# Kernel tuning notes

Hardware: AMD Instinct MI355X
Metric: run time of the kernel (lower is better)

The kernel has to match this reference:

```python
import jax, jax.numpy as jnp
import numpy as np

N_SRC = 50000
N_TGT = 50000
E = 320000
D = 256          # feature dim == hidden_channels
H = 256
OUT = 16
L = 2
P_DROP = 0.1
NEG_SLOPE = 0.01  # F.leaky_relu default


def _seg_mean(x, src_idx, dst_idx, n_dst):
    # gather source features along edges, mean-aggregate per destination (PyG SAGE default aggr='mean')
    msgs = x[src_idx]                                            # [E, D]
    s = jax.ops.segment_sum(msgs, dst_idx, num_segments=n_dst)   # [n_dst, D]
    cnt = jax.ops.segment_sum(jnp.ones((dst_idx.shape[0],), x.dtype), dst_idx, num_segments=n_dst)
    return s / jnp.maximum(cnt, 1.0)[:, None]


def _dropout(x, p, key):
    keep = jax.random.bernoulli(key, 1.0 - p, x.shape)
    return jnp.where(keep, x / (1.0 - p), jnp.zeros((), x.dtype))


def setup_inputs() -> dict:
    key = jax.random.key(0)
    ks = jax.random.split(key, 16)
    sc_in = 1.0 / np.sqrt(D)
    sc_h = 1.0 / np.sqrt(H)
    inp = {
        'x_source': jax.random.normal(ks[0], (N_SRC, D), jnp.float32),
        'x_target': jax.random.normal(ks[1], (N_TGT, D), jnp.float32),
        'ei_st': jax.random.randint(ks[2], (2, E), 0, N_SRC, jnp.int32),  # row0: source idx, row1: target idx
        'ei_ts': jax.random.randint(ks[3], (2, E), 0, N_TGT, jnp.int32),  # row0: target idx, row1: source idx
        # SAGEConv params per layer per relation; lin_l has bias, lin_r does not (PyG)
        'Wl_st': jax.random.normal(ks[4], (L, D, H), jnp.float32) * sc_in,
        'Wr_st': jax.random.normal(ks[5], (L, D, H), jnp.float32) * sc_in,
        'b_st': jnp.zeros((L, H), jnp.float32),
        'Wl_ts': jax.random.normal(ks[6], (L, D, H), jnp.float32) * sc_in,
        'Wr_ts': jax.random.normal(ks[7], (L, D, H), jnp.float32) * sc_in,
        'b_ts': jnp.zeros((L, H), jnp.float32),
        'Wout': jax.random.normal(ks[8], (H, OUT), jnp.float32) * sc_h,
        'bout': jnp.zeros((OUT,), jnp.float32),
    }
    return inp


def reference(x_source, x_target, ei_st, ei_ts, Wl_st, Wr_st, b_st, Wl_ts, Wr_ts, b_ts, Wout, bout):
    drop_key = jax.random.key(42)
    x_s, x_t = x_source, x_target
    for l in range(L):
        # relation ('source','edge','target'): messages source -> target
        m_t = _seg_mean(x_s, ei_st[0], ei_st[1], N_TGT)
        new_t = m_t @ Wl_st[l] + b_st[l] + x_t @ Wr_st[l]
        # relation ('target','rev_edge','source'): messages target -> source
        m_s = _seg_mean(x_t, ei_ts[0], ei_ts[1], N_SRC)
        new_s = m_s @ Wl_ts[l] + b_ts[l] + x_s @ Wr_ts[l]
        # leaky_relu + dropout (F.dropout default training=True)
        new_s = jnp.where(new_s >= 0, new_s, NEG_SLOPE * new_s)
        new_t = jnp.where(new_t >= 0, new_t, NEG_SLOPE * new_t)
        x_s = _dropout(new_s, P_DROP, jax.random.fold_in(drop_key, 2 * l))
        x_t = _dropout(new_t, P_DROP, jax.random.fold_in(drop_key, 2 * l + 1))
    return x_s @ Wout + bout  # [N_SRC, OUT]
```

## Files before the change

kernel.cpp:

```cpp
#include <hip/hip_runtime.h>
#include <stdint.h>

#define NSRC 50000
#define NTGT 50000
#define NE   320000
#define DIN  256
#define HID  256
#define DOUT 16

#define GBM 64
#define GBLK ((NSRC + GBM - 1) / GBM)
#define MASK_DW_PER (GBLK * 512)

typedef __attribute__((ext_vector_type(8))) short bf16x8;
typedef __attribute__((ext_vector_type(4))) float f32x4;
typedef __attribute__((ext_vector_type(4))) uint u32x4;

__device__ inline ushort f2b(float f) {
  uint32_t u = __float_as_uint(f);
  return (ushort)((u + 0x7FFFu + ((u >> 16) & 1u)) >> 16);
}
__device__ inline float b2f(ushort h) { return __uint_as_float(((uint32_t)h) << 16); }

typedef __attribute__((address_space(3))) uint32_t lds_u32_t;
typedef const __attribute__((address_space(1))) uint32_t glb_u32_t;
__device__ __forceinline__ void ld_lds16(const ushort* g, ushort* lds) {
  __builtin_amdgcn_global_load_lds((glb_u32_t*)g, (lds_u32_t*)lds, 16, 0, 0);
}

__host__ __device__ constexpr uint64_t tf2x32(uint32_t k0, uint32_t k1,
                                              uint32_t x0, uint32_t x1) {
  uint32_t ks2 = k0 ^ k1 ^ 0x1BD11BDAu;
  x0 += k0; x1 += k1;
#define TF_ROT(x, r) (((x) << (r)) | ((x) >> (32 - (r))))
#define TF_RND(r) { x0 += x1; x1 = TF_ROT(x1, r) ^ x0; }
  TF_RND(13) TF_RND(15) TF_RND(26) TF_RND(6)
  x0 += k1;  x1 += ks2 + 1u;
  TF_RND(17) TF_RND(29) TF_RND(16) TF_RND(24)
  x0 += ks2; x1 += k0 + 2u;
  TF_RND(13) TF_RND(15) TF_RND(26) TF_RND(6)
  x0 += k0;  x1 += k1 + 3u;
  TF_RND(17) TF_RND(29) TF_RND(16) TF_RND(24)
  x0 += k1;  x1 += ks2 + 4u;
  TF_RND(13) TF_RND(15) TF_RND(26) TF_RND(6)
  x0 += ks2; x1 += k0 + 5u;
#undef TF_RND
#undef TF_ROT
  return (uint64_t(x0) << 32) | uint64_t(x1);
}

constexpr uint64_t FOLD[4] = {
  tf2x32(0u, 42u, 0u, 0u),
  tf2x32(0u, 42u, 0u, 1u),
  tf2x32(0u, 42u, 0u, 2u),
  tf2x32(0u, 42u, 0u, 3u),
};

__device__ __forceinline__ void mask_word(uint32_t* __restrict__ masks, int d) {
  int g = d / MASK_DW_PER;
  int w = d - g * MASK_DW_PER;
  int gt = w >> 1, half = w & 1;
  int gblk = gt >> 8, gtid = gt & 255;
  int wave = gtid >> 6, lane = gtid & 63;
  int q = lane >> 4, r = lane & 15;
  uint64_t fk = (g == 0) ? FOLD[1] : (g == 1 ? FOLD[0] : FOLD[2]);
  uint32_t kk0 = (uint32_t)(fk >> 32), kk1 = (uint32_t)fk;
  int mbase = gblk * GBM;
  uint32_t mword = 0;
#pragma unroll
  for (int bb = 0; bb < 32; ++bb) {
    int s = half * 32 + bb;
    int si = s >> 4, se = (s >> 2) & 3, sj = s & 3;
    uint32_t rowg = (uint32_t)(mbase + si * 16 + q * 4 + se);
    uint32_t colg = (uint32_t)(wave * 64 + sj * 16 + r);
    uint64_t rr = tf2x32(kk0, kk1, 0u, rowg * 256u + colg);
    uint32_t bits = (uint32_t)(rr >> 32) ^ (uint32_t)rr;
    mword |= (((bits >> 9) < 7549747u) ? 1u : 0u) << bb;
  }
  masks[d] = mword;
}

#define NB_CVT  25000
#define NB_W    96
#define NB_HIST 2500
#define PREP_T  (NB_CVT + NB_W + NB_HIST)

struct PrepArgs {
  const float *xs, *xt;
  ushort *oxs, *oxt;
  const float* wsrc[6];
  ushort* wdst[6];
  const int *ei_a, *ei_b;
  int *cur_a, *cur_b;
};

__global__ __launch_bounds__(256) void prep_kernel(PrepArgs p) {
  __shared__ ushort tile[64][65];
  int blk = (int)(((long long)blockIdx.x * 97) % PREP_T);
  int tid = threadIdx.x;
  if (blk < NB_CVT) {
    const float* in = blk < (NB_CVT / 2) ? p.xs : p.xt;
    ushort* out = blk < (NB_CVT / 2) ? p.oxs : p.oxt;
    int i = (blk % (NB_CVT / 2)) * 256 + tid;
    float4 v = ((const float4*)in)[i];
    ushort4 o;
    o.x = f2b(v.x); o.y = f2b(v.y); o.z = f2b(v.z); o.w = f2b(v.w);
    ((ushort4*)out)[i] = o;
    return;
  }
  blk -= NB_CVT;
  if (blk < NB_W) {
    const float* W = p.wsrc[blk >> 4];
    ushort* Wt = p.wdst[blk >> 4];
    int ktile = (blk >> 2) & 3, ntile = blk & 3;
#pragma unroll
    for (int rep = 0; rep < 16; ++rep) {
      int lin = rep * 256 + tid;
      int kk = lin >> 6, nn = lin & 63;
      tile[nn][kk] = f2b(W[(size_t)(ktile * 64 + kk) * 256 + ntile * 64 + nn]);
    }
    __syncthreads();
#pragma unroll
    for (int rep = 0; rep < 16; ++rep) {
      int lin = rep * 256 + tid;
      int nn = lin >> 6, kk = lin & 63;
      Wt[(size_t)(ntile * 64 + nn) * 256 + ktile * 64 + kk] = tile[nn][kk];
    }
    return;
  }
  blk -= NB_W;
  const int* ei = blk < (NB_HIST / 2) ? p.ei_a : p.ei_b;
  int* cur = blk < (NB_HIST / 2) ? p.cur_a : p.cur_b;
  int e = (blk % (NB_HIST / 2)) * 256 + tid;
  if (e < NE) atomicAdd(cur + ei[NE + e], 1);
}

#define SB 1024
__global__ __launch_bounds__(SB) void scan_partial(const int* __restrict__ cur_a,
                                                   const int* __restrict__ cur_b,
                                                   int* __restrict__ bsum,
                                                   int n, int nbPer) {
  __shared__ int red[SB];
  int b = blockIdx.x;
  const int* cnt = b < nbPer ? cur_a : cur_b;
  int i = (b % nbPer) * SB + threadIdx.x;
  red[threadIdx.x] = (i < n) ? cnt[i] : 0;
  __syncthreads();
  for (int d = SB / 2; d > 0; d >>= 1) {
    if (threadIdx.x < d) red[threadIdx.x] += red[threadIdx.x + d];
    __syncthreads();
  }
  if (threadIdx.x == 0) bsum[b] = red[0];
}

__global__ __launch_bounds__(128) void scan_base(int* __restrict__ bsum, int nbPer) {
  __shared__ int buf[2][64];
  int half = threadIdx.x >> 6;
  int t = threadIdx.x & 63;
  buf[half][t] = (t < nbPer) ? bsum[half * nbPer + t] : 0;
  __syncthreads();
  for (int d = 1; d < 64; d <<= 1) {
    int v = (t >= d) ? buf[half][t - d] : 0;
    __syncthreads();
    buf[half][t] += v;
    __syncthreads();
  }
  if (t < nbPer) bsum[half * nbPer + t] = (t == 0) ? 0 : buf[half][t - 1];
}

__global__ __launch_bounds__(SB) void scan_final(int* __restrict__ cur_a,
                                                 int* __restrict__ cur_b,
                                                 int* __restrict__ offs_a,
                                                 int* __restrict__ offs_b,
                                                 const int* __restrict__ bsum,
                                                 int n, int nbPer) {
  __shared__ int part[SB];
  int b = blockIdx.x;
  bool first = b < nbPer;
  int* cur = first ? cur_a : cur_b;
  int* offs = first ? offs_a : offs_b;
  int i = (b % nbPer) * SB + threadIdx.x;
  int v = (i < n) ? cur[i] : 0;
  part[threadIdx.x] = v;
  __syncthreads();
  for (int d = 1; d < SB; d <<= 1) {
    int tv = (threadIdx.x >= d) ? part[threadIdx.x - d] : 0;
    __syncthreads();
    part[threadIdx.x] += tv;
    __syncthreads();
  }
  int excl = part[threadIdx.x] - v + bsum[b];
  if (i < n) {
    offs[i] = excl;
    cur[i] = 0;
  }
  if (i == n - 1) offs[n] = excl + v;
}

__global__ __launch_bounds__(256) void csr_fill2(const int* __restrict__ ei_a,
                                                 const int* __restrict__ ei_b,
                                                 const int* __restrict__ offs_a,
                                                 const int* __restrict__ offs_b,
                                                 int* __restrict__ cur_a,
                                                 int* __restrict__ cur_b,
                                                 int* __restrict__ adj_a,
                                                 int* __restrict__ adj_b,
                                                 int nE, int nbPer) {
  int blk = blockIdx.x;
  bool first = blk < nbPer;
  const int* ei = first ? ei_a : ei_b;
  const int* offs = first ? offs_a : offs_b;
  int* cur = first ? cur_a : cur_b;
  int* adj = first ? adj_a : adj_b;
  int e = (blk % nbPer) * 256 + threadIdx.x;
  if (e >= nE) return;
  int dst = ei[nE + e];
  int pos = atomicAdd(cur + dst, 1);
  adj[offs[dst] + pos] = ei[e];
}

__device__ __forceinline__ void gather_row8(const ushort* __restrict__ x,
                                            const int* __restrict__ offs,
                                            const int* __restrict__ adj,
                                            ushort* __restrict__ m,
                                            int row, int lane) {
  int start = offs[row], end = offs[row + 1];
  float a0 = 0.f, a1 = 0.f, a2 = 0.f, a3 = 0.f;
  float a4 = 0.f, a5 = 0.f, a6 = 0.f, a7 = 0.f;
  const ushort* xb = x + lane * 8;
  int e = start;
  for (; e + 3 < end; e += 4) {
    int s0 = adj[e], s1 = adj[e + 1], s2 = adj[e + 2], s3 = adj[e + 3];
    u32x4 v0 = *(const u32x4*)(xb + (size_t)s0 * DIN);
    u32x4 v1 = *(const u32x4*)(xb + (size_t)s1 * DIN);
    u32x4 v2 = *(const u32x4*)(xb + (size_t)s2 * DIN);
    u32x4 v3 = *(const u32x4*)(xb + (size_t)s3 * DIN);
    const ushort* u;
    u = (const ushort*)&v0;
    a0 += b2f(u[0]); a1 += b2f(u[1]); a2 += b2f(u[2]); a3 += b2f(u[3]);
    a4 += b2f(u[4]); a5 += b2f(u[5]); a6 += b2f(u[6]); a7 += b2f(u[7]);
    u = (const ushort*)&v1;
    a0 += b2f(u[0]); a1 += b2f(u[1]); a2 += b2f(u[2]); a3 += b2f(u[3]);
    a4 += b2f(u[4]); a5 += b2f(u[5]); a6 += b2f(u[6]); a7 += b2f(u[7]);
    u = (const ushort*)&v2;
    a0 += b2f(u[0]); a1 += b2f(u[1]); a2 += b2f(u[2]); a3 += b2f(u[3]);
    a4 += b2f(u[4]); a5 += b2f(u[5]); a6 += b2f(u[6]); a7 += b2f(u[7]);
    u = (const ushort*)&v3;
    a0 += b2f(u[0]); a1 += b2f(u[1]); a2 += b2f(u[2]); a3 += b2f(u[3]);
    a4 += b2f(u[4]); a5 += b2f(u[5]); a6 += b2f(u[6]); a7 += b2f(u[7]);
  }
  for (; e < end; ++e) {
    int s = adj[e];
    u32x4 v = *(const u32x4*)(xb + (size_t)s * DIN);
    const ushort* u = (const ushort*)&v;
    a0 += b2f(u[0]); a1 += b2f(u[1]); a2 += b2f(u[2]); a3 += b2f(u[3]);
    a4 += b2f(u[4]); a5 += b2f(u[5]); a6 += b2f(u[6]); a7 += b2f(u[7]);
  }
  float inv = 1.0f / fmaxf((float)(end - start), 1.0f);
  ushort o[8];
  o[0] = f2b(a0 * inv); o[1] = f2b(a1 * inv); o[2] = f2b(a2 * inv); o[3] = f2b(a3 * inv);
  o[4] = f2b(a4 * inv); o[5] = f2b(a5 * inv); o[6] = f2b(a6 * inv); o[7] = f2b(a7 * inv);
  *(u32x4*)(m + (size_t)row * DIN + lane * 8) = *(const u32x4*)o;
}

#define GG_GB 6250
#define G2_MASKB (2 * MASK_DW_PER / 256)
#define GM_T (GG_GB + G2_MASKB)

__global__ __launch_bounds__(256) void gather_mask_h(
    const ushort* __restrict__ x, const int* __restrict__ offs,
    const int* __restrict__ adj, ushort* __restrict__ m,
    uint32_t* __restrict__ masks, int nRows) {
  int blk = (int)(((long long)blockIdx.x * 97) % GM_T);
  int tid = threadIdx.x;
  if (blk >= GG_GB) {
    mask_word(masks, (blk - GG_GB) * 256 + tid);
    return;
  }
  int row = blk * 8 + (tid >> 5);
  if (row < nRows) gather_row8(x, offs, adj, m, row, tid & 31);
}

__device__ __forceinline__ void gemm_kloop(
    int bid, const ushort* __restrict__ A1, const ushort* __restrict__ A2,
    const ushort* __restrict__ W1t, const ushort* __restrict__ W2t,
    int M, ushort* sA, ushort* sB, f32x4 acc[4][4]) {
  const int tid = threadIdx.x;
  const int wave = tid >> 6, lane = tid & 63;
  const int q = lane >> 4, r = lane & 15;
  const int mbase = bid * GBM;

  const int arow = tid >> 2;
  const int akc = (tid & 3) * 8;
  const int agrow = min(mbase + arow, M - 1);
  const ushort* a1p = A1 + (size_t)agrow * DIN + akc;
  const ushort* a2p = A2 + (size_t)agrow * DIN + akc;
  const ushort* w1b = W1t + (size_t)arow * DIN + akc;
  const ushort* w2b = W2t + (size_t)arow * DIN + akc;
  ushort* ldsA0 = sA + wave * 512;
  ushort* ldsA1 = sA + 2048 + wave * 512;

#pragma unroll
  for (int t = 0; t < 8; ++t) {
    const int kt = t * 32;
    __syncthreads();
    ld_lds16(a1p + kt, ldsA0);
    ld_lds16(a2p + kt, ldsA1);
#pragma unroll
    for (int c = 0; c < 4; ++c) {
      ld_lds16(w1b + c * (64 * DIN) + kt, sB + c * 2048 + wave * 512);
      ld_lds16(w2b + c * (64 * DIN) + kt, sB + 8192 + c * 2048 + wave * 512);
    }
    __syncthreads();
#pragma unroll
    for (int ph = 0; ph < 2; ++ph) {
      bf16x8 af[4], bfr[4];
#pragma unroll
      for (int i = 0; i < 4; ++i)
        af[i] = *(const bf16x8*)&sA[ph * 2048 + (i * 16 + r) * 32 + q * 8];
#pragma unroll
      for (int j = 0; j < 4; ++j)
        bfr[j] = *(const bf16x8*)&sB[ph * 8192 + (wave * 64 + j * 16 + r) * 32 + q * 8];
#pragma unroll
      for (int i = 0; i < 4; ++i)
#pragma unroll
        for (int j = 0; j < 4; ++j)
          acc[i][j] = __builtin_amdgcn_mfma_f32_16x16x32_bf16(af[i], bfr[j],
                                                              acc[i][j], 0, 0, 0);
    }
  }
}

__device__ __forceinline__ void gemm_body(
    int bid, const ushort* __restrict__ A1, const ushort* __restrict__ A2,
    const ushort* __restrict__ W1t, const ushort* __restrict__ W2t,
    const float* __restrict__ bias, const uint2* __restrict__ mk,
    ushort* __restrict__ C, int M, ushort* sA, ushort* sB) {
  const int tid = threadIdx.x;
  const int wave = tid >> 6, lane = tid & 63;
  const int q = lane >> 4, r = lane & 15;
  const int mbase = bid * GBM;
  const uint2 km = mk[bid * 256 + tid];

  f32x4 acc[4][4] = {};
  gemm_kloop(bid, A1, A2, W1t, W2t, M, sA, sB, acc);

  float bj[4];
#pragma unroll
  for (int j = 0; j < 4; ++j) bj[j] = bias[wave * 64 + j * 16 + r];
#pragma unroll
  for (int i = 0; i < 4; ++i) {
#pragma unroll
    for (int e = 0; e < 4; ++e) {
      int rowg = mbase + i * 16 + q * 4 + e;
      if (rowg >= M) continue;
#pragma unroll
      for (int j = 0; j < 4; ++j) {
        const int s = i * 16 + e * 4 + j;
        int colg = wave * 64 + j * 16 + r;
        float v = acc[i][j][e] + bj[j];
        v = v >= 0.0f ? v : 0.01f * v;
        uint32_t keep = ((s < 32 ? km.x >> s : km.y >> (s - 32)) & 1u);
        v = keep ? v * (1.0f / 0.9f) : 0.0f;
        C[(size_t)rowg * HID + colg] = f2b(v);
      }
    }
  }
}

__global__ __launch_bounds__(256, 4) void gemm_dual_mfma(
    const ushort* __restrict__ A1, const ushort* __restrict__ A2,
    const ushort* __restrict__ W1t, const ushort* __restrict__ W2t,
    const float* __restrict__ bias, const uint2* __restrict__ mk,
    ushort* __restrict__ C, int M) {
  __shared__ ushort sA[2][GBM * 32];
  __shared__ ushort sB[2][HID * 32];
  gemm_body(blockIdx.x, A1, A2, W1t, W2t, bias, mk, C, M, &sA[0][0], &sB[0][0]);
}

#define G1_T (GBLK + GG_GB)

__global__ __launch_bounds__(256, 4) void gemm1_gather(
    const ushort* __restrict__ A1, const ushort* __restrict__ A2,
    const ushort* __restrict__ W1t, const ushort* __restrict__ W2t,
    const float* __restrict__ bias, const uint2* __restrict__ mk,
    ushort* __restrict__ C, int M,
    const ushort* __restrict__ gx, const int* __restrict__ goffs,
    const int* __restrict__ gadj, ushort* __restrict__ gm, int gRows) {
  __shared__ ushort sA[2][GBM * 32];
  __shared__ ushort sB[2][HID * 32];
  int blk = (int)(((long long)blockIdx.x * 101) % G1_T);
  if (blk < GBLK) {
    gemm_body(blk, A1, A2, W1t, W2t, bias, mk, C, M, &sA[0][0], &sB[0][0]);
  } else {
    int row = (blk - GBLK) * 8 + (threadIdx.x >> 5);
    if (row < gRows) gather_row8(gx, goffs, gadj, gm, row, threadIdx.x & 31);
  }
}

#define GG_MASKB (MASK_DW_PER / 256)
#define GG_T  (GBLK + GG_GB + GG_MASKB)

__global__ __launch_bounds__(256, 4) void gemm_gather(
    const ushort* __restrict__ A1, const ushort* __restrict__ A2,
    const ushort* __restrict__ W1t, const ushort* __restrict__ W2t,
    const float* __restrict__ bias, const uint2* __restrict__ mk,
    ushort* __restrict__ C, int M,
    const ushort* __restrict__ gx, const int* __restrict__ goffs,
    const int* __restrict__ gadj, ushort* __restrict__ gm, int gRows,
    uint32_t* __restrict__ masks) {
  __shared__ ushort sA[2][GBM * 32];
  __shared__ ushort sB[2][HID * 32];
  int blk = (int)(((long long)blockIdx.x * 101) % GG_T);
  if (blk < GBLK) {
    gemm_body(blk, A1, A2, W1t, W2t, bias, mk, C, M, &sA[0][0], &sB[0][0]);
  } else if (blk < GBLK + GG_GB) {
    int row = (blk - GBLK) * 8 + (threadIdx.x >> 5);
    if (row < gRows) gather_row8(gx, goffs, gadj, gm, row, threadIdx.x & 31);
  } else {
    mask_word(masks,
              2 * MASK_DW_PER + (blk - GBLK - GG_GB) * 256 + (int)threadIdx.x);
  }
}

__global__ __launch_bounds__(256) void out_gemm_h(const ushort* __restrict__ X,
                                                  const float* __restrict__ Wout,
                                                  const float* __restrict__ bout,
                                                  float* __restrict__ C, int M) {
  __shared__ float sW[DIN * DOUT];
  int tid = threadIdx.x;
#pragma unroll
  for (int i = 0; i < (DIN * DOUT) / 256; ++i) sW[i * 256 + tid] = Wout[i * 256 + tid];
  __syncthreads();
  int rr = tid >> 4, c = tid & 15;
  int row = blockIdx.x * 16 + rr;
  if (row >= M) return;
  float acc = bout[c];
  const ushort* xp = X + (size_t)row * DIN;
  for (int k = 0; k < DIN; k += 8) {
    uint4 u = *(const uint4*)(xp + k);
    const ushort* us = (const ushort*)&u;
#pragma unroll
    for (int t = 0; t < 8; ++t) acc += b2f(us[t]) * sW[(k + t) * DOUT + c];
  }
  C[(size_t)row * DOUT + c] = acc;
}

extern "C" void kernel_launch(void* const* d_in, const int* in_sizes, int n_in,
                              void* d_out, int out_size, void* d_ws, size_t ws_size,
                              hipStream_t stream) {
  const float* x_source = (const float*)d_in[0];
  const float* x_target = (const float*)d_in[1];
  const int* ei_st = (const int*)d_in[2];
  const int* ei_ts = (const int*)d_in[3];
  const float* Wl_st = (const float*)d_in[4];
  const float* Wr_st = (const float*)d_in[5];
  const float* b_st  = (const float*)d_in[6];
  const float* Wl_ts = (const float*)d_in[7];
  const float* Wr_ts = (const float*)d_in[8];
  const float* b_ts  = (const float*)d_in[9];
  const float* Wout  = (const float*)d_in[10];
  const float* bout  = (const float*)d_in[11];
  float* out = (float*)d_out;

  const size_t F = (size_t)NSRC * DIN;
  const size_t WM = (size_t)DIN * HID;
  const int nbScan = (NSRC + SB - 1) / SB;
  const size_t intCount = (NTGT + 1) + (NSRC + 1) + 2 * NE + NTGT + NSRC +
                          2 * nbScan + 3 * MASK_DW_PER;
  const size_t need = (5 * F + 6 * WM) * sizeof(ushort) + intCount * sizeof(int);
  if (ws_size < need) return;

  ushort* xs0h = (ushort*)d_ws;
  ushort* xt0h = xs0h + F;
  ushort* B0h  = xt0h + F;
  ushort* B1h  = B0h + F;
  ushort* B2h  = B1h + F;
  ushort* wt0  = B2h + F;
  ushort* wt1  = wt0 + WM;
  ushort* wt2  = wt1 + WM;
  ushort* wt3  = wt2 + WM;
  ushort* wt4  = wt3 + WM;
  ushort* wt5  = wt4 + WM;
  int* ip      = (int*)(wt5 + WM);
  int* offs_st = ip;
  int* offs_ts = offs_st + NTGT + 1;
  int* adj_st  = offs_ts + NSRC + 1;
  int* adj_ts  = adj_st + NE;
  int* cur_t   = adj_ts + NE;
  int* cur_s   = cur_t + NTGT;
  int* bsum    = cur_s + NSRC;
  uint32_t* masks = (uint32_t*)(bsum + 2 * nbScan);

  const int EB = (NE + 255) / 256;

  (void)hipMemsetAsync(cur_t, 0, (NTGT + NSRC) * sizeof(int), stream);
  PrepArgs pa;
  pa.xs = x_source; pa.xt = x_target; pa.oxs = xs0h; pa.oxt = xt0h;
  pa.wsrc[0] = Wl_st;      pa.wdst[0] = wt0;
  pa.wsrc[1] = Wr_st;      pa.wdst[1] = wt1;
  pa.wsrc[2] = Wl_ts;      pa.wdst[2] = wt2;
  pa.wsrc[3] = Wr_ts;      pa.wdst[3] = wt3;
  pa.wsrc[4] = Wl_ts + WM; pa.wdst[4] = wt4;
  pa.wsrc[5] = Wr_ts + WM; pa.wdst[5] = wt5;
  pa.ei_a = ei_st; pa.ei_b = ei_ts;
  pa.cur_a = cur_t; pa.cur_b = cur_s;
  prep_kernel<<<PREP_T, 256, 0, stream>>>(pa);

  scan_partial<<<2 * nbScan, SB, 0, stream>>>(cur_t, cur_s, bsum, NTGT, nbScan);
  scan_base<<<1, 128, 0, stream>>>(bsum, nbScan);
  scan_final<<<2 * nbScan, SB, 0, stream>>>(cur_t, cur_s, offs_st, offs_ts,
                                            bsum, NTGT, nbScan);
  csr_fill2<<<2 * EB, 256, 0, stream>>>(ei_st, ei_ts, offs_st, offs_ts,
                                        cur_t, cur_s, adj_st, adj_ts, NE, EB);

  gather_mask_h<<<GM_T, 256, 0, stream>>>(xs0h, offs_st, adj_st, B0h,
                                          masks, NTGT);

  gemm1_gather<<<G1_T, 256, 0, stream>>>(
      B0h, xt0h, wt0, wt1, b_st, (const uint2*)(masks), B2h, NTGT,
      xt0h, offs_ts, adj_ts, B1h, NSRC);

  gemm_gather<<<GG_T, 256, 0, stream>>>(
      B1h, xs0h, wt2, wt3, b_ts, (const uint2*)(masks + MASK_DW_PER), B0h, NSRC,
      B2h, offs_ts, adj_ts, xt0h, NSRC, masks);

  gemm_dual_mfma<<<GBLK, 256, 0, stream>>>(
      xt0h, B0h, wt4, wt5, b_ts + HID, (const uint2*)(masks + 2 * MASK_DW_PER),
      B2h, NSRC);

  out_gemm_h<<<(NSRC + 15) / 16, 256, 0, stream>>>(B2h, Wout, bout, out, NSRC);
}
```

Measured before the change: 442.2 us.

## Fuse neighbor gather and dropout mask generation into SAGE GEMM kernels

Each GEMM block now gathers and mean-aggregates its own 64 rows into a global bounce buffer, then runs the dual GEMM on it. It also computes its dropout mask bits inline instead of reading a precomputed mask buffer. Layer-1 dropout for the target side is skipped, since the final output depends only on source features. This cuts the launches from four to two, removes the mask buffer, and lets the two layer-1 relations run in one grid. The cost is that blocks now serialize gather latency before the MFMA loop, and the gather no longer overlaps GEMM work done by other blocks within a launch.

```diff
diff --git a/kernel.cpp b/kernel.cpp
--- a/kernel.cpp
+++ b/kernel.cpp
@@ -10,7 +10,6 @@
 
 #define GBM 64
 #define GBLK ((NSRC + GBM - 1) / GBM)
-#define MASK_DW_PER (GBLK * 512)
 
 typedef __attribute__((ext_vector_type(8))) short bf16x8;
 typedef __attribute__((ext_vector_type(4))) float f32x4;
@@ -56,28 +55,24 @@
   tf2x32(0u, 42u, 0u, 3u),
 };
 
-__device__ __forceinline__ void mask_word(uint32_t* __restrict__ masks, int d) {
-  int g = d / MASK_DW_PER;
-  int w = d - g * MASK_DW_PER;
-  int gt = w >> 1, half = w & 1;
-  int gblk = gt >> 8, gtid = gt & 255;
-  int wave = gtid >> 6, lane = gtid & 63;
-  int q = lane >> 4, r = lane & 15;
+__device__ __forceinline__ uint2 mask_pair(int g, int bid, int wave, int q, int r) {
   uint64_t fk = (g == 0) ? FOLD[1] : (g == 1 ? FOLD[0] : FOLD[2]);
   uint32_t kk0 = (uint32_t)(fk >> 32), kk1 = (uint32_t)fk;
-  int mbase = gblk * GBM;
-  uint32_t mword = 0;
-#pragma unroll
-  for (int bb = 0; bb < 32; ++bb) {
-    int s = half * 32 + bb;
+  int mbase = bid * GBM;
+  uint32_t kmx = 0, kmy = 0;
+#pragma unroll 2
+  for (int s = 0; s < 64; ++s) {
     int si = s >> 4, se = (s >> 2) & 3, sj = s & 3;
     uint32_t rowg = (uint32_t)(mbase + si * 16 + q * 4 + se);
     uint32_t colg = (uint32_t)(wave * 64 + sj * 16 + r);
     uint64_t rr = tf2x32(kk0, kk1, 0u, rowg * 256u + colg);
     uint32_t bits = (uint32_t)(rr >> 32) ^ (uint32_t)rr;
-    mword |= (((bits >> 9) < 7549747u) ? 1u : 0u) << bb;
-  }
-  masks[d] = mword;
+    uint32_t b = ((bits >> 9) < 7549747u) ? 1u : 0u;
+    if (s < 32) kmx |= b << s;
+    else        kmy |= b << (s - 32);
+  }
+  uint2 km; km.x = kmx; km.y = kmy;
+  return km;
 }
 
 #define NB_CVT  25000
@@ -219,10 +214,10 @@
   adj[offs[dst] + pos] = ei[e];
 }
 
-__device__ __forceinline__ void gather_row8(const ushort* __restrict__ x,
+__device__ __forceinline__ void gather_row8(const ushort* x,
                                             const int* __restrict__ offs,
                                             const int* __restrict__ adj,
-                                            ushort* __restrict__ m,
+                                            ushort* m,
                                             int row, int lane) {
   int start = offs[row], end = offs[row + 1];
   float a0 = 0.f, a1 = 0.f, a2 = 0.f, a3 = 0.f;
@@ -263,26 +258,8 @@
   *(u32x4*)(m + (size_t)row * DIN + lane * 8) = *(const u32x4*)o;
 }
 
-#define GG_GB 6250
-#define G2_MASKB (2 * MASK_DW_PER / 256)
-#define GM_T (GG_GB + G2_MASKB)
-
-__global__ __launch_bounds__(256) void gather_mask_h(
-    const ushort* __restrict__ x, const int* __restrict__ offs,
-    const int* __restrict__ adj, ushort* __restrict__ m,
-    uint32_t* __restrict__ masks, int nRows) {
-  int blk = (int)(((long long)blockIdx.x * 97) % GM_T);
-  int tid = threadIdx.x;
-  if (blk >= GG_GB) {
-    mask_word(masks, (blk - GG_GB) * 256 + tid);
-    return;
-  }
-  int row = blk * 8 + (tid >> 5);
-  if (row < nRows) gather_row8(x, offs, adj, m, row, tid & 31);
-}
-
 __device__ __forceinline__ void gemm_kloop(
-    int bid, const ushort* __restrict__ A1, const ushort* __restrict__ A2,
+    int bid, const ushort* A1, const ushort* __restrict__ A2,
     const ushort* __restrict__ W1t, const ushort* __restrict__ W2t,
     int M, ushort* sA, ushort* sB, f32x4 acc[4][4]) {
   const int tid = threadIdx.x;
@@ -331,23 +308,34 @@
   }
 }
 
-__device__ __forceinline__ void gemm_body(
-    int bid, const ushort* __restrict__ A1, const ushort* __restrict__ A2,
+__device__ __forceinline__ void gemm_fused_body(
+    int bid, int g, const ushort* gsrc,
+    const int* __restrict__ goffs, const int* __restrict__ gadj,
+    ushort* bounce, const ushort* __restrict__ A2,
     const ushort* __restrict__ W1t, const ushort* __restrict__ W2t,
-    const float* __restrict__ bias, const uint2* __restrict__ mk,
-    ushort* __restrict__ C, int M, ushort* sA, ushort* sB) {
+    const float* __restrict__ bias, ushort* C, int M,
+    ushort* sA, ushort* sB) {
   const int tid = threadIdx.x;
   const int wave = tid >> 6, lane = tid & 63;
   const int q = lane >> 4, r = lane & 15;
   const int mbase = bid * GBM;
-  const uint2 km = mk[bid * 256 + tid];
+
+#pragma unroll
+  for (int pass = 0; pass < 8; ++pass) {
+    int row = mbase + pass * 8 + (tid >> 5);
+    if (row < M) gather_row8(gsrc, goffs, gadj, bounce, row, tid & 31);
+  }
+  __syncthreads();
 
   f32x4 acc[4][4] = {};
-  gemm_kloop(bid, A1, A2, W1t, W2t, M, sA, sB, acc);
+  gemm_kloop(bid, bounce, A2, W1t, W2t, M, sA, sB, acc);
 
   float bj[4];
 #pragma unroll
   for (int j = 0; j < 4; ++j) bj[j] = bias[wave * 64 + j * 16 + r];
+
+  const uint2 km = mask_pair(g, bid, wave, q, r);
+
 #pragma unroll
   for (int i = 0; i < 4; ++i) {
 #pragma unroll
@@ -368,59 +356,38 @@
   }
 }
 
-__global__ __launch_bounds__(256, 4) void gemm_dual_mfma(
-    const ushort* __restrict__ A1, const ushort* __restrict__ A2,
-    const ushort* __restrict__ W1t, const ushort* __restrict__ W2t,
-    const float* __restrict__ bias, const uint2* __restrict__ mk,
-    ushort* __restrict__ C, int M) {
+#define FA_T (2 * GBLK)
+
+__global__ __launch_bounds__(256, 4) void gemm_fused12(
+    const ushort* __restrict__ xs, const ushort* __restrict__ xt,
+    const int* __restrict__ offs_st, const int* __restrict__ adj_st,
+    const int* __restrict__ offs_ts, const int* __restrict__ adj_ts,
+    const ushort* __restrict__ wt0, const ushort* __restrict__ wt1,
+    const ushort* __restrict__ wt2, const ushort* __restrict__ wt3,
+    const float* __restrict__ b_st, const float* __restrict__ b_ts,
+    ushort* B0, ushort* B2, int M) {
   __shared__ ushort sA[2][GBM * 32];
   __shared__ ushort sB[2][HID * 32];
-  gemm_body(blockIdx.x, A1, A2, W1t, W2t, bias, mk, C, M, &sA[0][0], &sB[0][0]);
-}
-
-#define G1_T (GBLK + GG_GB)
-
-__global__ __launch_bounds__(256, 4) void gemm1_gather(
-    const ushort* __restrict__ A1, const ushort* __restrict__ A2,
-    const ushort* __restrict__ W1t, const ushort* __restrict__ W2t,
-    const float* __restrict__ bias, const uint2* __restrict__ mk,
-    ushort* __restrict__ C, int M,
-    const ushort* __restrict__ gx, const int* __restrict__ goffs,
-    const int* __restrict__ gadj, ushort* __restrict__ gm, int gRows) {
+  int blk = (int)(((long long)blockIdx.x * 101) % FA_T);
+  if (blk < GBLK) {
+    gemm_fused_body(blk, 0, xs, offs_st, adj_st, B2, xt, wt0, wt1, b_st,
+                    B2, M, &sA[0][0], &sB[0][0]);
+  } else {
+    gemm_fused_body(blk - GBLK, 1, xt, offs_ts, adj_ts, B0, xs, wt2, wt3, b_ts,
+                    B0, M, &sA[0][0], &sB[0][0]);
+  }
+}
+
+__global__ __launch_bounds__(256, 4) void gemm_fused3(
+    const ushort* __restrict__ t1,
+    const int* __restrict__ offs_ts, const int* __restrict__ adj_ts,
+    ushort* B1, const ushort* __restrict__ s1,
+    const ushort* __restrict__ wt4, const ushort* __restrict__ wt5,
+    const float* __restrict__ bias, ushort* C, int M) {
   __shared__ ushort sA[2][GBM * 32];
   __shared__ ushort sB[2][HID * 32];
-  int blk = (int)(((long long)blockIdx.x * 101) % G1_T);
-  if (blk < GBLK) {
-    gemm_body(blk, A1, A2, W1t, W2t, bias, mk, C, M, &sA[0][0], &sB[0][0]);
-  } else {
-    int row = (blk - GBLK) * 8 + (threadIdx.x >> 5);
-    if (row < gRows) gather_row8(gx, goffs, gadj, gm, row, threadIdx.x & 31);
-  }
-}
-
-#define GG_MASKB (MASK_DW_PER / 256)
-#define GG_T  (GBLK + GG_GB + GG_MASKB)
-
-__global__ __launch_bounds__(256, 4) void gemm_gather(
-    const ushort* __restrict__ A1, const ushort* __restrict__ A2,
-    const ushort* __restrict__ W1t, const ushort* __restrict__ W2t,
-    const float* __restrict__ bias, const uint2* __restrict__ mk,
-    ushort* __restrict__ C, int M,
-    const ushort* __restrict__ gx, const int* __restrict__ goffs,
-    const int* __restrict__ gadj, ushort* __restrict__ gm, int gRows,
-    uint32_t* __restrict__ masks) {
-  __shared__ ushort sA[2][GBM * 32];
-  __shared__ ushort sB[2][HID * 32];
-  int blk = (int)(((long long)blockIdx.x * 101) % GG_T);
-  if (blk < GBLK) {
-    gemm_body(blk, A1, A2, W1t, W2t, bias, mk, C, M, &sA[0][0], &sB[0][0]);
-  } else if (blk < GBLK + GG_GB) {
-    int row = (blk - GBLK) * 8 + (threadIdx.x >> 5);
-    if (row < gRows) gather_row8(gx, goffs, gadj, gm, row, threadIdx.x & 31);
-  } else {
-    mask_word(masks,
-              2 * MASK_DW_PER + (blk - GBLK - GG_GB) * 256 + (int)threadIdx.x);
-  }
+  gemm_fused_body(blockIdx.x, 2, t1, offs_ts, adj_ts, B1, s1, wt4, wt5, bias,
+                  C, M, &sA[0][0], &sB[0][0]);
 }
 
 __global__ __launch_bounds__(256) void out_gemm_h(const ushort* __restrict__ X,
@@ -467,7 +434,7 @@
   const size_t WM = (size_t)DIN * HID;
   const int nbScan = (NSRC + SB - 1) / SB;
   const size_t intCount = (NTGT + 1) + (NSRC + 1) + 2 * NE + NTGT + NSRC +
-                          2 * nbScan + 3 * MASK_DW_PER;
+                          2 * nbScan;
   const size_t need = (5 * F + 6 * WM) * sizeof(ushort) + intCount * sizeof(int);
   if (ws_size < need) return;
 
@@ -490,7 +457,6 @@
   int* cur_t   = adj_ts + NE;
   int* cur_s   = cur_t + NTGT;
   int* bsum    = cur_s + NSRC;
-  uint32_t* masks = (uint32_t*)(bsum + 2 * nbScan);
 
   const int EB = (NE + 255) / 256;
 
@@ -514,20 +480,12 @@
   csr_fill2<<<2 * EB, 256, 0, stream>>>(ei_st, ei_ts, offs_st, offs_ts,
                                         cur_t, cur_s, adj_st, adj_ts, NE, EB);
 
-  gather_mask_h<<<GM_T, 256, 0, stream>>>(xs0h, offs_st, adj_st, B0h,
-                                          masks, NTGT);
-
-  gemm1_gather<<<G1_T, 256, 0, stream>>>(
-      B0h, xt0h, wt0, wt1, b_st, (const uint2*)(masks), B2h, NTGT,
-      xt0h, offs_ts, adj_ts, B1h, NSRC);
-
-  gemm_gather<<<GG_T, 256, 0, stream>>>(
-      B1h, xs0h, wt2, wt3, b_ts, (const uint2*)(masks + MASK_DW_PER), B0h, NSRC,
-      B2h, offs_ts, adj_ts, xt0h, NSRC, masks);
-
-  gemm_dual_mfma<<<GBLK, 256, 0, stream>>>(
-      xt0h, B0h, wt4, wt5, b_ts + HID, (const uint2*)(masks + 2 * MASK_DW_PER),
-      B2h, NSRC);
-
-  out_gemm_h<<<(NSRC + 15) / 16, 256, 0, stream>>>(B2h, Wout, bout, out, NSRC);
-}
+  gemm_fused12<<<FA_T, 256, 0, stream>>>(
+      xs0h, xt0h, offs_st, adj_st, offs_ts, adj_ts,
+      wt0, wt1, wt2, wt3, b_st, b_ts, B0h, B2h, NSRC);
+
+  gemm_fused3<<<GBLK, 256, 0, stream>>>(
+      B2h, offs_ts, adj_ts, B1h, B0h, wt4, wt5, b_ts + HID, xs0h, NSRC);
+
+  out_gemm_h<<<(NSRC + 15) / 16, 256, 0, stream>>>(xs0h, Wout, bout, out, NSRC);
+}
```

After: 814.9 us. +84.3%, slower.
